# Optimization experiments

Measured on AMD Instinct MI355X. Metric: run time of the kernel, lower is better.

## Reference

```python
import jax, jax.numpy as jnp
import numpy as np
import math

EMBED = 1024
HEADS = 16
HEAD_DIM = EMBED // HEADS


def setup_inputs() -> dict:
    key = jax.random.key(0)
    ks = jax.random.split(key, 9)
    B, S = 2, 2048
    query = jax.random.normal(ks[0], (B, S, EMBED), dtype=jnp.float32)
    key_t = jax.random.normal(ks[1], (B, S, EMBED), dtype=jnp.float32)
    value = jax.random.normal(ks[2], (B, S, EMBED), dtype=jnp.float32)
    mask = jax.random.randint(ks[3], (B, 1, S, S), 0, 2, dtype=jnp.int32)
    # nn.Linear(head_dim, head_dim, bias=False) weights: [out, in]
    sc = 1.0 / math.sqrt(HEAD_DIM)
    Wq = jax.random.uniform(ks[4], (HEAD_DIM, HEAD_DIM), jnp.float32, -sc, sc)
    Wk = jax.random.uniform(ks[5], (HEAD_DIM, HEAD_DIM), jnp.float32, -sc, sc)
    Wv = jax.random.uniform(ks[6], (HEAD_DIM, HEAD_DIM), jnp.float32, -sc, sc)
    so = 1.0 / math.sqrt(EMBED)
    Wo = jax.random.uniform(ks[7], (EMBED, EMBED), jnp.float32, -so, so)
    bo = jax.random.uniform(ks[8], (EMBED,), jnp.float32, -so, so)
    return {"query": query, "key": key_t, "value": value, "mask": mask,
            "Wq": Wq, "Wk": Wk, "Wv": Wv, "Wo": Wo, "bo": bo}


def reference(query, key, value, mask, Wq, Wk, Wv, Wo, bo):
    B, Sq, E = query.shape
    Sk = key.shape[1]
    H, D = HEADS, HEAD_DIM
    # Faithful raw reshape into heads (as in the torch source, no transpose)
    q = query.reshape(B, H, Sq, D)
    k = key.reshape(B, H, Sk, D)
    v = value.reshape(B, H, Sk, D)
    # per-head_dim Linear (bias-free): x @ W.T
    Q = jnp.einsum('bhsd,ed->bhse', q, Wq)
    K = jnp.einsum('bhsd,ed->bhse', k, Wk)
    V = jnp.einsum('bhsd,ed->bhse', v, Wv)
    scores = jnp.einsum('bhqd,bhkd->bhqk', Q, K)  # [B,H,Sq,Sk]
    scores = jnp.where(mask == 0, jnp.float32(-1e20), scores)
    # NOTE: source divides by sqrt(embed_size), not sqrt(head_dim)
    attn = jax.nn.softmax(scores / jnp.float32(math.sqrt(E)), axis=-1)
    out = jnp.einsum('bhqk,bhkd->bhqd', attn, V).reshape(B, Sq, H * D)
    return out @ Wo.T + bo
```

## Files before the change

### kernel.cpp

```cpp
#include <hip/hip_runtime.h>

typedef __attribute__((ext_vector_type(8))) short short8;
typedef __attribute__((ext_vector_type(4))) float f32x4;
typedef __attribute__((ext_vector_type(2))) int int2v;
typedef __attribute__((ext_vector_type(4))) int int4v;

__device__ __forceinline__ short f2bf(float f) {
  unsigned u = __builtin_bit_cast(unsigned, f);
  u += 0x7fff + ((u >> 16) & 1);
  return (short)(u >> 16);
}

__device__ __forceinline__ int pk2bf(float lo, float hi) {
#if defined(__gfx950__) && __has_builtin(__builtin_amdgcn_cvt_pk_bf16_f32)
  typedef __attribute__((ext_vector_type(2))) __bf16 bf16x2;
  bf16x2 v = __builtin_amdgcn_cvt_pk_bf16_f32(lo, hi);
  return __builtin_bit_cast(int, v);
#else
  return (int)(unsigned short)(short)f2bf(lo) | (((int)f2bf(hi)) << 16);
#endif
}

__device__ __forceinline__ int pktr(float lo, float hi) {
  return (int)(__builtin_bit_cast(unsigned, lo) >> 16) |
         (int)(__builtin_bit_cast(unsigned, hi) & 0xffff0000u);
}

__device__ __forceinline__ short8 pack8(f32x4 a, f32x4 b) {
  int4v t;
  t.x = pk2bf(a[0], a[1]);
  t.y = pk2bf(a[2], a[3]);
  t.z = pk2bf(b[0], b[1]);
  t.w = pk2bf(b[2], b[3]);
  return __builtin_bit_cast(short8, t);
}

__device__ __forceinline__ float fand(float p, int m) {
  return __builtin_bit_cast(float, __builtin_bit_cast(int, p) & m);
}

__device__ __forceinline__ int bmask(unsigned w, int bit) {
#if __has_builtin(__builtin_amdgcn_sbfe)
  return __builtin_amdgcn_sbfe((int)w, bit, 1);
#else
  return ((int)(w << (31 - bit))) >> 31;
#endif
}

__device__ __forceinline__ float fexp2(float x) {
#if __has_builtin(__builtin_amdgcn_exp2f)
  return __builtin_amdgcn_exp2f(x);
#else
  return exp2f(x);
#endif
}

__device__ __forceinline__ void glds16(const short* g, short* lbase, int lane) {
#if __has_builtin(__builtin_amdgcn_global_load_lds)
  __builtin_amdgcn_global_load_lds(
      (const __attribute__((address_space(1))) unsigned int*)g,
      (__attribute__((address_space(3))) unsigned int*)lbase, 16, 0, 0);
#else
  *(short8*)(lbase + lane * 8) = *(const short8*)g;
#endif
}

__global__ __launch_bounds__(256) void prep(const float* __restrict__ q,
                                            const float* __restrict__ k,
                                            const float* __restrict__ v,
                                            const float* __restrict__ Wq,
                                            const float* __restrict__ Wk,
                                            const float* __restrict__ Wv,
                                            const float* __restrict__ Wo,
                                            const int* __restrict__ mask,
                                            short* __restrict__ Qp,
                                            short* __restrict__ Kp,
                                            short* __restrict__ Vtp,
                                            short* __restrict__ Wob,
                                            unsigned* __restrict__ mmod) {
  const int bid = blockIdx.x;
  const int tid = threadIdx.x;

  if (bid >= 4096) {
    const int mb = bid - 4096;
    const int kp = mb & 15, bq = mb >> 4;
    const int b_ = bq >> 5, q64 = bq & 31;
    const int wv = tid >> 6, qd = (tid >> 4) & 3, m16_ = tid & 15;
    unsigned d = 0;
#pragma unroll
    for (int hb = 0; hb < 2; ++hb) {
      const int* mr = mask + b_ * 4194304 + (q64 * 64 + wv * 16 + m16_) * 2048 +
                      (kp * 2 + hb) * 64 + qd * 4;
#pragma unroll
      for (int grp = 0; grp < 4; ++grp)
#pragma unroll
        for (int r = 0; r < 4; ++r)
          if (mr[grp * 16 + r] != 0) d |= 1u << (hb * 16 + grp * 4 + r);
    }
    mmod[mb * 256 + tid] = d;
    return;
  }
  if (bid >= 3072) {
    const int i = ((bid - 3072) * 256 + tid) * 4;
    const f32x4 x = *(const f32x4*)&Wo[i];
    int2v o;
    o.x = pk2bf(x[0], x[1]);
    o.y = pk2bf(x[2], x[3]);
    *(int2v*)&Wob[i] = o;
    return;
  }

  __shared__ short xt[64][72];
  __shared__ short ot[64][72];
  const int mode = bid >> 10;
  const int bt = bid & 1023;
  const float* X;
  const float* W;
  float scale;
  if (mode == 0) { X = q; W = Wq; scale = 0.045084220f; }
  else if (mode == 1) { X = k; W = Wk; scale = 1.0f; }
  else { X = v; W = Wv; scale = 1.0f; }

  const int r0 = bt * 64;
  const int row = tid >> 2, seg = (tid & 3) * 16;
  const f32x4* xs = (const f32x4*)(X + (r0 + row) * 64 + seg);
  const f32x4 x0 = xs[0], x1 = xs[1], x2 = xs[2], x3 = xs[3];
  *(short8*)&xt[row][seg] = pack8(x0, x1);
  *(short8*)&xt[row][seg + 8] = pack8(x2, x3);
  __syncthreads();

  const int lane = tid & 63, wave = tid >> 6;
  const int m16 = lane & 15, quad = lane >> 4;

  const short8 a0 = *(const short8*)&xt[wave * 16 + m16][quad * 8];
  const short8 a1 = *(const short8*)&xt[wave * 16 + m16][32 + quad * 8];

  f32x4 acc[4];
#pragma unroll
  for (int nt = 0; nt < 4; ++nt) {
    const f32x4* wp0 = (const f32x4*)&W[(nt * 16 + m16) * 64 + quad * 8];
    const f32x4* wp1 = (const f32x4*)&W[(nt * 16 + m16) * 64 + 32 + quad * 8];
    const short8 b0 = pack8(wp0[0], wp0[1]);
    const short8 b1 = pack8(wp1[0], wp1[1]);
    f32x4 z = (f32x4){0.f, 0.f, 0.f, 0.f};
    z = __builtin_amdgcn_mfma_f32_16x16x32_bf16(a0, b0, z, 0, 0, 0);
    z = __builtin_amdgcn_mfma_f32_16x16x32_bf16(a1, b1, z, 0, 0, 0);
    acc[nt] = z;
  }

  if (mode != 2) {
#pragma unroll
    for (int nt = 0; nt < 4; ++nt)
#pragma unroll
      for (int r = 0; r < 4; ++r)
        ot[wave * 16 + quad * 4 + r][nt * 16 + m16] = f2bf(acc[nt][r] * scale);
  } else {
#pragma unroll
    for (int nt = 0; nt < 4; ++nt)
#pragma unroll
      for (int r = 0; r < 4; ++r)
        ot[nt * 16 + m16][quad * 8 + (wave & 1) * 4 + r + (wave >> 1) * 32] =
            f2bf(acc[nt][r]);
  }
  __syncthreads();

  const int orow = tid >> 2, opart = tid & 3;
  if (mode != 2) {
    short* dst = (mode == 0 ? Qp : Kp) + (r0 + orow) * 64 + opart * 16;
    *(short8*)&dst[0] = *(const short8*)&ot[orow][opart * 16];
    *(short8*)&dst[8] = *(const short8*)&ot[orow][opart * 16 + 8];
  } else {
    const int bh = r0 >> 11, s0 = r0 & 2047;
    short* dst = Vtp + bh * 131072 + orow * 2048 + s0 + opart * 16;
    *(short8*)&dst[0] = *(const short8*)&ot[orow][opart * 16];
    *(short8*)&dst[8] = *(const short8*)&ot[orow][opart * 16 + 8];
  }
}

__global__ __launch_bounds__(256) void flash64r(const short* __restrict__ Qp,
                                                const short* __restrict__ Kp,
                                                const short* __restrict__ Vt,
                                                const unsigned* __restrict__ mmod,
                                                short* __restrict__ Ob) {
  __shared__ __attribute__((aligned(16))) short kt0[4096];
  __shared__ __attribute__((aligned(16))) short kt1[4096];
  __shared__ __attribute__((aligned(16))) short vt0[4096];
  __shared__ __attribute__((aligned(16))) short vt1[4096];
  const int tid = threadIdx.x;
  const int bid = blockIdx.x;
  const int local = bid >> 3;
  const int qblk = local & 31;
  const int bh = (bid & 7) * 4 + (local >> 5);
  const int q0 = qblk << 6;
  const int b = bh >> 4;
  const short* Qh = Qp + bh * 131072;
  const short* Kh = Kp + bh * 131072;
  const short* Vh = Vt + bh * 131072;
  const int lane = tid & 63, wave = tid >> 6;
  const int m16 = lane & 15, quad = lane >> 4;
  const int srow = lane >> 3, sj = (lane & 7) ^ srow;
  const int koff = m16 * 128 + ((quad ^ (m16 & 7)) * 16);
  const unsigned* mq = mmod + ((b * 32 + qblk) * 16) * 256 + wave * 64 + quad * 16 + m16;

  const short onebf = (short)0x3F80;
  const short8 ones = (short8){onebf, onebf, onebf, onebf, onebf, onebf, onebf, onebf};

  short8 aq[2];
#pragma unroll
  for (int h = 0; h < 2; ++h)
    aq[h] = *(const short8*)&Qh[(q0 + wave * 16 + m16) * 64 + h * 32 + quad * 8];

  f32x4 oaccL = (f32x4){0.f, 0.f, 0.f, 0.f};
  f32x4 oacc[4];
#pragma unroll
  for (int dt = 0; dt < 4; ++dt) oacc[dt] = (f32x4){0.f, 0.f, 0.f, 0.f};

  auto stage = [&](short* ktb, short* vtb, int ka) {
#pragma unroll
    for (int t = 0; t < 2; ++t) {
      const int crow = wave * 16 + t * 8;
      glds16(Kh + (ka * 64 + crow + srow) * 64 + sj * 8, ktb + crow * 64, lane);
      glds16(Vh + (crow + srow) * 2048 + ka * 64 + sj * 8, vtb + crow * 64, lane);
    }
  };

  auto compute = [&](const short* ktp, const short* vtp, unsigned mw, int bb) {
    const char* ktb = (const char*)ktp;
    const char* vtb = (const char*)vtp;
    f32x4 s[4];
    __builtin_amdgcn_s_setprio(1);
#pragma unroll
    for (int grp = 0; grp < 4; ++grp) {
      const int o0 = grp * 2048 + koff;
      const short8 kb0 = *(const short8*)(ktb + o0);
      const short8 kb1 = *(const short8*)(ktb + (o0 ^ 64));
      f32x4 z = (f32x4){0.f, 0.f, 0.f, 0.f};
      z = __builtin_amdgcn_mfma_f32_16x16x32_bf16(kb0, aq[0], z, 0, 0, 0);
      z = __builtin_amdgcn_mfma_f32_16x16x32_bf16(kb1, aq[1], z, 0, 0, 0);
      s[grp] = z;
    }
    __builtin_amdgcn_s_setprio(0);

    float p[4][4];
#pragma unroll
    for (int grp = 0; grp < 4; ++grp)
#pragma unroll
      for (int r = 0; r < 4; ++r)
        p[grp][r] = fand(fexp2(s[grp][r]), bmask(mw, bb + grp * 4 + r));

    int4v t0, t1;
    t0.x = pktr(p[0][0], p[0][1]);
    t0.y = pktr(p[0][2], p[0][3]);
    t0.z = pktr(p[1][0], p[1][1]);
    t0.w = pktr(p[1][2], p[1][3]);
    t1.x = pktr(p[2][0], p[2][1]);
    t1.y = pktr(p[2][2], p[2][3]);
    t1.z = pktr(p[3][0], p[3][1]);
    t1.w = pktr(p[3][2], p[3][3]);
    const short8 ap0 = __builtin_bit_cast(short8, t0);
    const short8 ap1 = __builtin_bit_cast(short8, t1);

    __builtin_amdgcn_s_setprio(1);
    oaccL = __builtin_amdgcn_mfma_f32_16x16x32_bf16(ap0, ones, oaccL, 0, 0, 0);
    oaccL = __builtin_amdgcn_mfma_f32_16x16x32_bf16(ap1, ones, oaccL, 0, 0, 0);
#pragma unroll
    for (int dt = 0; dt < 4; ++dt) {
      const int o0 = dt * 2048 + koff;
      const short8 vb0 = *(const short8*)(vtb + o0);
      const short8 vb1 = *(const short8*)(vtb + (o0 ^ 64));
      f32x4 z = oacc[dt];
      z = __builtin_amdgcn_mfma_f32_16x16x32_bf16(ap0, vb0, z, 0, 0, 0);
      z = __builtin_amdgcn_mfma_f32_16x16x32_bf16(ap1, vb1, z, 0, 0, 0);
      oacc[dt] = z;
    }
    __builtin_amdgcn_s_setprio(0);
  };

  unsigned mw = mq[0];
  stage(kt0, vt0, 0);
  stage(kt1, vt1, 1);

  for (int kk = 0; kk < 15; ++kk) {
    const unsigned mwn = mq[(kk + 1) * 256];
    asm volatile("s_waitcnt vmcnt(5)" ::: "memory");
    __builtin_amdgcn_s_barrier();
    compute(kt0, vt0, mw, 0);
    __builtin_amdgcn_s_barrier();
    stage(kt0, vt0, 2 * kk + 2);
    asm volatile("s_waitcnt vmcnt(5)" ::: "memory");
    __builtin_amdgcn_s_barrier();
    compute(kt1, vt1, mw, 16);
    __builtin_amdgcn_s_barrier();
    stage(kt1, vt1, 2 * kk + 3);
    mw = mwn;
  }
  asm volatile("s_waitcnt vmcnt(4)" ::: "memory");
  __builtin_amdgcn_s_barrier();
  compute(kt0, vt0, mw, 0);
  asm volatile("s_waitcnt vmcnt(0)" ::: "memory");
  __builtin_amdgcn_s_barrier();
  compute(kt1, vt1, mw, 16);

  float linv[4];
#pragma unroll
  for (int r = 0; r < 4; ++r) linv[r] = 1.0f / oaccL[r];

  char* const ptB = (char*)kt0;
#pragma unroll
  for (int r = 0; r < 4; ++r) {
    const int row = wave * 16 + quad * 4 + r;
#pragma unroll
    for (int dt = 0; dt < 4; ++dt)
      *(short*)(ptB + row * 128 + ((dt * 32 + m16 * 2) ^ ((row & 7) << 4))) =
          f2bf(oacc[dt][r] * linv[r]);
  }
  asm volatile("s_waitcnt lgkmcnt(0)" ::: "memory");

  const int orow = lane >> 2, opart = lane & 3;
  const int prow = wave * 16 + orow;
  const int oswz = (orow & 7) << 4;
  short* og = Ob + (bh * 2048 + q0 + prow) * 64 + opart * 16;
  *(short8*)&og[0] = *(const short8*)(ptB + prow * 128 + ((opart * 32) ^ oswz));
  *(short8*)&og[8] = *(const short8*)(ptB + prow * 128 + ((opart * 32 + 16) ^ oswz));
}

__global__ __launch_bounds__(256) void outproj(const short* __restrict__ Ob,
                                               const short* __restrict__ Wob,
                                               const float* __restrict__ bo,
                                               float* __restrict__ out) {
  __shared__ __attribute__((aligned(16))) short at0[4096];
  __shared__ __attribute__((aligned(16))) short at1[4096];
  __shared__ __attribute__((aligned(16))) short bt0[8192];
  __shared__ __attribute__((aligned(16))) short bt1[8192];
  const int tid = threadIdx.x;
  const int bid = blockIdx.x;
  const int ct = bid >> 6, rt = bid & 63;
  const int r0 = rt * 64, c0 = ct * 128;
  const int lane = tid & 63, wave = tid >> 6;
  const int mr = (wave >> 1) * 32, nc = (wave & 1) * 64;
  const int m16 = lane & 15, quad = lane >> 4;
  const int srow = lane >> 3, sj = (lane & 7) ^ srow;
  const int mswz = (m16 & 7) << 4;

  f32x4 acc[2][4];
#pragma unroll
  for (int mt = 0; mt < 2; ++mt)
#pragma unroll
    for (int nt = 0; nt < 4; ++nt) acc[mt][nt] = (f32x4){0.f, 0.f, 0.f, 0.f};

  auto stageK = [&](short* atb, short* btb, int kc) {
#pragma unroll
    for (int t = 0; t < 2; ++t) {
      const int crow = wave * 16 + t * 8;
      glds16(Ob + (r0 + crow + srow) * 1024 + kc * 64 + sj * 8, atb + crow * 64, lane);
    }
#pragma unroll
    for (int t = 0; t < 4; ++t) {
      const int crow = wave * 32 + t * 8;
      glds16(Wob + (c0 + crow + srow) * 1024 + kc * 64 + sj * 8, btb + crow * 64, lane);
    }
  };

  auto computeK = [&](const short* atp, const short* btp) {
    const char* atB = (const char*)atp;
    const char* btB = (const char*)btp;
#pragma unroll
    for (int kh = 0; kh < 2; ++kh) {
      short8 af[2], bf[4];
#pragma unroll
      for (int i = 0; i < 2; ++i)
        af[i] = *(const short8*)(atB + (mr + i * 16 + m16) * 128 +
                                 ((kh * 64 + quad * 16) ^ mswz));
#pragma unroll
      for (int j = 0; j < 4; ++j)
        bf[j] = *(const short8*)(btB + (nc + j * 16 + m16) * 128 +
                                 ((kh * 64 + quad * 16) ^ mswz));
      __builtin_amdgcn_s_setprio(1);
#pragma unroll
      for (int mt = 0; mt < 2; ++mt)
#pragma unroll
        for (int nt = 0; nt < 4; ++nt)
          acc[mt][nt] = __builtin_amdgcn_mfma_f32_16x16x32_bf16(af[mt], bf[nt],
                                                                acc[mt][nt], 0, 0, 0);
      __builtin_amdgcn_s_setprio(0);
    }
  };

  stageK(at0, bt0, 0);
  stageK(at1, bt1, 1);
  for (int kc = 0; kc < 14; ++kc) {
    short* atb = (kc & 1) ? at1 : at0;
    short* btb = (kc & 1) ? bt1 : bt0;
    asm volatile("s_waitcnt vmcnt(6)" ::: "memory");
    __builtin_amdgcn_s_barrier();
    computeK(atb, btb);
    __builtin_amdgcn_s_barrier();
    stageK(atb, btb, kc + 2);
  }
  asm volatile("s_waitcnt vmcnt(6)" ::: "memory");
  __builtin_amdgcn_s_barrier();
  computeK(at0, bt0);
  asm volatile("s_waitcnt vmcnt(0)" ::: "memory");
  __builtin_amdgcn_s_barrier();
  computeK(at1, bt1);

#pragma unroll
  for (int nt = 0; nt < 4; ++nt) {
    const int col = c0 + nc + nt * 16 + m16;
    const float bias = bo[col];
#pragma unroll
    for (int mt = 0; mt < 2; ++mt)
#pragma unroll
      for (int rr2 = 0; rr2 < 4; ++rr2)
        out[(r0 + mr + mt * 16 + quad * 4 + rr2) * 1024 + col] = acc[mt][nt][rr2] + bias;
  }
}

extern "C" void kernel_launch(void* const* d_in, const int* in_sizes, int n_in,
                              void* d_out, int out_size, void* d_ws, size_t ws_size,
                              hipStream_t stream) {
  const float* query = (const float*)d_in[0];
  const float* key = (const float*)d_in[1];
  const float* value = (const float*)d_in[2];
  const int* mask = (const int*)d_in[3];
  const float* Wq = (const float*)d_in[4];
  const float* Wk = (const float*)d_in[5];
  const float* Wv = (const float*)d_in[6];
  const float* Wo = (const float*)d_in[7];
  const float* bo = (const float*)d_in[8];
  float* out = (float*)d_out;

  char* ws = (char*)d_ws;
  short* Qp = (short*)(ws);
  short* Kp = (short*)(ws + 8388608);
  short* Vt = (short*)(ws + 16777216);
  short* Ob = (short*)(ws + 25165824);
  short* Wob = (short*)(ws + 41943040);
  unsigned* mmod = (unsigned*)(ws + 44564480);

  prep<<<5120, 256, 0, stream>>>(query, key, value, Wq, Wk, Wv, Wo, mask,
                                 Qp, Kp, Vt, Wob, mmod);
  flash64r<<<1024, 256, 0, stream>>>(Qp, Kp, Vt, mmod, Ob);
  outproj<<<512, 256, 0, stream>>>(Ob, Wob, bo, out);
}
```

Before: 218.4 us.

## Split prep kernel and coalesce mask bit-packing through shared memory

```diff
diff --git a/kernel.cpp b/kernel.cpp
--- a/kernel.cpp
+++ b/kernel.cpp
@@ -22,8 +22,13 @@
 }
 
 __device__ __forceinline__ int pktr(float lo, float hi) {
+#if __has_builtin(__builtin_amdgcn_perm)
+  return (int)__builtin_amdgcn_perm(__builtin_bit_cast(unsigned, hi),
+                                    __builtin_bit_cast(unsigned, lo), 0x07060302u);
+#else
   return (int)(__builtin_bit_cast(unsigned, lo) >> 16) |
          (int)(__builtin_bit_cast(unsigned, hi) & 0xffff0000u);
+#endif
 }
 
 __device__ __forceinline__ short8 pack8(f32x4 a, f32x4 b) {
@@ -65,50 +70,17 @@
 #endif
 }
 
-__global__ __launch_bounds__(256) void prep(const float* __restrict__ q,
-                                            const float* __restrict__ k,
-                                            const float* __restrict__ v,
-                                            const float* __restrict__ Wq,
-                                            const float* __restrict__ Wk,
-                                            const float* __restrict__ Wv,
-                                            const float* __restrict__ Wo,
-                                            const int* __restrict__ mask,
-                                            short* __restrict__ Qp,
-                                            short* __restrict__ Kp,
-                                            short* __restrict__ Vtp,
-                                            short* __restrict__ Wob,
-                                            unsigned* __restrict__ mmod) {
+__global__ __launch_bounds__(256) void projqkv(const float* __restrict__ q,
+                                               const float* __restrict__ k,
+                                               const float* __restrict__ v,
+                                               const float* __restrict__ Wq,
+                                               const float* __restrict__ Wk,
+                                               const float* __restrict__ Wv,
+                                               short* __restrict__ Qp,
+                                               short* __restrict__ Kp,
+                                               short* __restrict__ Vtp) {
   const int bid = blockIdx.x;
   const int tid = threadIdx.x;
-
-  if (bid >= 4096) {
-    const int mb = bid - 4096;
-    const int kp = mb & 15, bq = mb >> 4;
-    const int b_ = bq >> 5, q64 = bq & 31;
-    const int wv = tid >> 6, qd = (tid >> 4) & 3, m16_ = tid & 15;
-    unsigned d = 0;
-#pragma unroll
-    for (int hb = 0; hb < 2; ++hb) {
-      const int* mr = mask + b_ * 4194304 + (q64 * 64 + wv * 16 + m16_) * 2048 +
-                      (kp * 2 + hb) * 64 + qd * 4;
-#pragma unroll
-      for (int grp = 0; grp < 4; ++grp)
-#pragma unroll
-        for (int r = 0; r < 4; ++r)
-          if (mr[grp * 16 + r] != 0) d |= 1u << (hb * 16 + grp * 4 + r);
-    }
-    mmod[mb * 256 + tid] = d;
-    return;
-  }
-  if (bid >= 3072) {
-    const int i = ((bid - 3072) * 256 + tid) * 4;
-    const f32x4 x = *(const f32x4*)&Wo[i];
-    int2v o;
-    o.x = pk2bf(x[0], x[1]);
-    o.y = pk2bf(x[2], x[3]);
-    *(int2v*)&Wob[i] = o;
-    return;
-  }
 
   __shared__ short xt[64][72];
   __shared__ short ot[64][72];
@@ -175,6 +147,58 @@
     *(short8*)&dst[0] = *(const short8*)&ot[orow][opart * 16];
     *(short8*)&dst[8] = *(const short8*)&ot[orow][opart * 16 + 8];
   }
+}
+
+__global__ __launch_bounds__(256) void maskwo(const int* __restrict__ mask,
+                                              const float* __restrict__ Wo,
+                                              short* __restrict__ Wob,
+                                              unsigned* __restrict__ mmod) {
+  const int bid = blockIdx.x;
+  const int tid = threadIdx.x;
+
+  if (bid >= 1024) {
+    const int i = ((bid - 1024) * 256 + tid) * 4;
+    const f32x4 x = *(const f32x4*)&Wo[i];
+    int2v o;
+    o.x = pk2bf(x[0], x[1]);
+    o.y = pk2bf(x[2], x[3]);
+    *(int2v*)&Wob[i] = o;
+    return;
+  }
+
+  __shared__ __attribute__((aligned(16))) unsigned char mbits[8192];
+  const int mb = bid;
+  const int kp = mb & 15, bq = mb >> 4;
+  const int b_ = bq >> 5, q64 = bq & 31;
+  const int* msrc = mask + b_ * 4194304 + q64 * 64 * 2048 + kp * 128;
+
+#pragma unroll
+  for (int i = 0; i < 8; ++i) {
+    const int idx = tid + i * 256;
+    const int row = idx >> 5;
+    const int col = (idx * 4) & 127;
+    const int4v x = *(const int4v*)(msrc + row * 2048 + col);
+    const unsigned w = (unsigned)x.x | ((unsigned)x.y << 8) |
+                       ((unsigned)x.z << 16) | ((unsigned)x.w << 24);
+    *(unsigned*)(mbits + row * 128 + (col ^ ((row & 7) << 4))) = w;
+  }
+  __syncthreads();
+
+  const int wv = tid >> 6, qd = (tid >> 4) & 3, m16_ = tid & 15;
+  const int row = wv * 16 + m16_;
+  const int swz = (row & 7) << 4;
+  const unsigned char* rb = mbits + row * 128;
+  unsigned d = 0;
+#pragma unroll
+  for (int hb = 0; hb < 2; ++hb)
+#pragma unroll
+    for (int grp = 0; grp < 4; ++grp) {
+      const unsigned w =
+          *(const unsigned*)(rb + ((hb * 64 + grp * 16 + qd * 4) ^ swz));
+      const unsigned nib = (((w & 0x01010101u) * 0x01020408u) >> 24) & 0xFu;
+      d |= nib << (hb * 16 + grp * 4);
+    }
+  mmod[mb * 256 + tid] = d;
 }
 
 __global__ __launch_bounds__(256) void flash64r(const short* __restrict__ Qp,
@@ -200,6 +224,7 @@
   const int m16 = lane & 15, quad = lane >> 4;
   const int srow = lane >> 3, sj = (lane & 7) ^ srow;
   const int koff = m16 * 128 + ((quad ^ (m16 & 7)) * 16);
+  const int koffx = koff ^ 64;
   const unsigned* mq = mmod + ((b * 32 + qblk) * 16) * 256 + wave * 64 + quad * 16 + m16;
 
   const short onebf = (short)0x3F80;
@@ -225,15 +250,16 @@
   };
 
   auto compute = [&](const short* ktp, const short* vtp, unsigned mw, int bb) {
-    const char* ktb = (const char*)ktp;
-    const char* vtb = (const char*)vtp;
+    const char* kb_lo = (const char*)ktp + koff;
+    const char* kb_hi = (const char*)ktp + koffx;
+    const char* vb_lo = (const char*)vtp + koff;
+    const char* vb_hi = (const char*)vtp + koffx;
     f32x4 s[4];
     __builtin_amdgcn_s_setprio(1);
 #pragma unroll
     for (int grp = 0; grp < 4; ++grp) {
-      const int o0 = grp * 2048 + koff;
-      const short8 kb0 = *(const short8*)(ktb + o0);
-      const short8 kb1 = *(const short8*)(ktb + (o0 ^ 64));
+      const short8 kb0 = *(const short8*)(kb_lo + grp * 2048);
+      const short8 kb1 = *(const short8*)(kb_hi + grp * 2048);
       f32x4 z = (f32x4){0.f, 0.f, 0.f, 0.f};
       z = __builtin_amdgcn_mfma_f32_16x16x32_bf16(kb0, aq[0], z, 0, 0, 0);
       z = __builtin_amdgcn_mfma_f32_16x16x32_bf16(kb1, aq[1], z, 0, 0, 0);
@@ -265,9 +291,8 @@
     oaccL = __builtin_amdgcn_mfma_f32_16x16x32_bf16(ap1, ones, oaccL, 0, 0, 0);
 #pragma unroll
     for (int dt = 0; dt < 4; ++dt) {
-      const int o0 = dt * 2048 + koff;
-      const short8 vb0 = *(const short8*)(vtb + o0);
-      const short8 vb1 = *(const short8*)(vtb + (o0 ^ 64));
+      const short8 vb0 = *(const short8*)(vb_lo + dt * 2048);
+      const short8 vb1 = *(const short8*)(vb_hi + dt * 2048);
       f32x4 z = oacc[dt];
       z = __builtin_amdgcn_mfma_f32_16x16x32_bf16(ap0, vb0, z, 0, 0, 0);
       z = __builtin_amdgcn_mfma_f32_16x16x32_bf16(ap1, vb1, z, 0, 0, 0);
@@ -438,8 +463,8 @@
   short* Wob = (short*)(ws + 41943040);
   unsigned* mmod = (unsigned*)(ws + 44564480);
 
-  prep<<<5120, 256, 0, stream>>>(query, key, value, Wq, Wk, Wv, Wo, mask,
-                                 Qp, Kp, Vt, Wob, mmod);
+  projqkv<<<3072, 256, 0, stream>>>(query, key, value, Wq, Wk, Wv, Qp, Kp, Vt);
+  maskwo<<<2048, 256, 0, stream>>>(mask, Wo, Wob, mmod);
   flash64r<<<1024, 256, 0, stream>>>(Qp, Kp, Vt, mmod, Ob);
   outproj<<<512, 256, 0, stream>>>(Ob, Wob, bo, out);
 }
```

Measured after the change: 219.5 us. No clear change (+0.5%).
